# Kernel tuning notes

Hardware: AMD Instinct MI355X
Metric: run time of the kernel (lower is better)

The kernel has to match this reference:

```python
import jax, jax.numpy as jnp
import numpy as np

B, N, H = 8, 2000, 64  # batch, num_nodes(=input_dim), hidden(num_gru_units)


def _laplacian_self_loop(a):
    # batched: norm = D^{-1/2} (A + I) D^{-1/2}
    m = a + jnp.eye(a.shape[-1], dtype=a.dtype)
    d_inv_sqrt = jnp.sum(m, axis=-1) ** -0.5  # (B, N)
    return d_inv_sqrt[..., :, None] * m * d_inv_sqrt[..., None, :]


def _graph_conv(inputs, hidden_flat, adj, windd, W2, b2, W3, b3, W, b, out_dim):
    b_, _, n = inputs.shape
    # dynamic wind-based adjacency
    wind_now = inputs[:, 2, :] * 360.0  # (B, N)
    direction = jnp.abs(windd[None, :, :] - wind_now[:, :, None])  # (B, N, N)
    direction = jnp.where(direction > 360.0, 180.0, direction)
    d1 = jnp.maximum(jnp.cos(direction * (jnp.pi / 180.0)), 0.0)
    a = d1 @ W2.T + b2 + (adj @ W3.T + b3)[None]  # (B, N, N)
    a1 = _laplacian_self_loop(jnp.maximum(a, 0.0))
    # graph conv: concat [x, h] then A @ [.] then Linear
    x = jnp.concatenate([inputs[:, 0, :, None], hidden_flat.reshape(b_, n, H)], axis=2)  # (B,N,H+1)
    y = jnp.einsum('bij,bjh->bih', a1, x) @ W.T + b  # (B, N, out_dim)
    return y.reshape(b_, n * out_dim)


def reference(inputs, hidden_state, adj, windd, W2, b2, W3, b3, W1a, b1a, W1b, b1b, Wca1, Wca2, Wsa):
    b_, _, n = inputs.shape
    conc = _graph_conv(inputs, hidden_state, adj, windd, W2, b2, W3, b3, W1a, b1a, 2 * H)
    conc = conc.reshape(b_, 2 * H, n)  # faithful reshape (input_dim == N)
    # --- channel attention (CBAM) ---
    avg = jnp.mean(conc, axis=2, keepdims=True)  # (B, 2H, 1)
    mx = jnp.max(conc, axis=2, keepdims=True)
    def fc(v):
        return jnp.einsum('oc,bcx->box', Wca2, jax.nn.relu(jnp.einsum('oc,bcx->box', Wca1, v)))
    ca = jax.nn.sigmoid(fc(avg) + fc(mx))  # (B, 2H, 1)
    conc = ca * conc
    # --- spatial attention ---
    s = jnp.stack([jnp.mean(conc, axis=1), jnp.max(conc, axis=1)], axis=1)  # (B, 2, N)
    sa = jax.lax.conv_general_dilated(s, Wsa, window_strides=(1,), padding=((3, 3),),
                                      dimension_numbers=('NCH', 'OIH', 'NCH'))  # (B,1,N)
    conc = jax.nn.sigmoid(sa) * conc
    # --- GRU gates ---
    conc = jax.nn.sigmoid(conc.reshape(b_, 2 * H * n))
    r, u = jnp.split(conc, 2, axis=1)  # each (B, N*H)
    c = jnp.tanh(_graph_conv(inputs, r * hidden_state, adj, windd, W2, b2, W3, b3, W1b, b1b, H))
    new_hidden_state = u * hidden_state + (1.0 - u) * c
    return new_hidden_state


def setup_inputs() -> dict:
    key = jax.random.key(0)
    ks = jax.random.split(key, 12)
    inputs = jax.random.uniform(ks[0], (B, 3, N), dtype=jnp.float32)
    hidden_state = jax.random.normal(ks[1], (B, N * H), dtype=jnp.float32) * 0.1
    adj = jax.random.uniform(ks[2], (N, N), dtype=jnp.float32)
    windd = jax.random.uniform(ks[3], (N, N), dtype=jnp.float32) * 360.0
    sN = 1.0 / np.sqrt(N)
    W2 = jax.random.normal(ks[4], (N, N), dtype=jnp.float32) * sN
    b2 = jnp.zeros((N,), jnp.float32)
    W3 = jax.random.normal(ks[5], (N, N), dtype=jnp.float32) * sN
    b3 = jnp.zeros((N,), jnp.float32)
    sI = 1.0 / np.sqrt(H + 1)
    W1a = jax.random.normal(ks[6], (2 * H, H + 1), dtype=jnp.float32) * sI
    b1a = jnp.ones((2 * H,), jnp.float32)  # bias=1.0 in graph_conv1
    W1b = jax.random.normal(ks[7], (H, H + 1), dtype=jnp.float32) * sI
    b1b = jnp.zeros((H,), jnp.float32)
    Wca1 = jax.random.normal(ks[8], (2 * H // 16, 2 * H), dtype=jnp.float32) * (1.0 / np.sqrt(2 * H))
    Wca2 = jax.random.normal(ks[9], (2 * H, 2 * H // 16), dtype=jnp.float32) * (1.0 / np.sqrt(2 * H // 16))
    Wsa = jax.random.normal(ks[10], (1, 2, 7), dtype=jnp.float32) * (1.0 / np.sqrt(14))
    return {'inputs': inputs, 'hidden_state': hidden_state, 'adj': adj, 'windd': windd,
            'W2': W2, 'b2': b2, 'W3': W3, 'b3': b3, 'W1a': W1a, 'b1a': b1a,
            'W1b': W1b, 'b1b': b1b, 'Wca1': Wca1, 'Wca2': Wca2, 'Wsa': Wsa}
```

## Files before the change

### kernel.cpp

```cpp
#include <hip/hip_runtime.h>

#define NN 2000
#define BB 8
#define P  2048
#define NKT 64

typedef __attribute__((ext_vector_type(8))) short bf16x8;
typedef __attribute__((ext_vector_type(4))) float f32x4;

__device__ __forceinline__ float sigf(float x) { return 1.0f / (1.0f + expf(-x)); }

__device__ __forceinline__ short f2bf(float x) {
    union { float f; unsigned u; } v; v.f = x;
    unsigned r = v.u + 0x7fffu + ((v.u >> 16) & 1u);
    return (short)(r >> 16);
}
__device__ __forceinline__ float bf2f(short h) {
    union { unsigned u; float f; } v; v.u = ((unsigned)(unsigned short)h) << 16; return v.f;
}

__device__ __forceinline__ void gl2lds16(const short* g, short* l) {
    __builtin_amdgcn_global_load_lds(
        (const __attribute__((address_space(1))) void*)g,
        (__attribute__((address_space(3))) void*)l, 16, 0, 0);
}

__global__ __launch_bounds__(256) void k_cvtW(
    const float* __restrict__ s0, const float* __restrict__ s1, const float* __restrict__ s2,
    short* __restrict__ d0, short* __restrict__ d1, short* __restrict__ d2)
{
    const int i = blockIdx.x, sel = blockIdx.y, t = threadIdx.x;
    const float* s = (sel == 0) ? s0 : (sel == 1) ? s1 : s2;
    short* d = ((sel == 0) ? d0 : (sel == 1) ? d1 : d2) + ((size_t)i) * P + t * 8;
    bf16x8 v;
#pragma unroll
    for (int e = 0; e < 8; ++e) v[e] = 0;
    if (i < NN && t < 250) {
        const float* p = s + (size_t)i * NN + t * 8;
        float4 x0 = *(const float4*)p;
        float4 x1 = *(const float4*)(p + 4);
        float a[8] = {x0.x,x0.y,x0.z,x0.w,x1.x,x1.y,x1.z,x1.w};
#pragma unroll
        for (int e = 0; e < 8; ++e) v[e] = f2bf(a[e]);
    }
    *(bf16x8*)d = v;
}

__global__ __launch_bounds__(256) void k_cvtD1(
    const float* __restrict__ windd, const float* __restrict__ inputs, short* __restrict__ d1bf)
{
    const int i = blockIdx.x, t = threadIdx.x;
    const bool live = (i < NN) && (t < 250);
    float a[8];
    if (live) {
        const float* p = windd + (size_t)i * NN + t * 8;
        float4 x0 = *(const float4*)p;
        float4 x1 = *(const float4*)(p + 4);
        a[0]=x0.x; a[1]=x0.y; a[2]=x0.z; a[3]=x0.w;
        a[4]=x1.x; a[5]=x1.y; a[6]=x1.z; a[7]=x1.w;
    }
#pragma unroll
    for (int b = 0; b < BB; ++b) {
        bf16x8 v;
#pragma unroll
        for (int e = 0; e < 8; ++e) v[e] = 0;
        if (live) {
            const float wn = inputs[(size_t)b * 3 * NN + 2 * NN + i] * 360.0f;
#pragma unroll
            for (int e = 0; e < 8; ++e) {
                float dd = fabsf(a[e] - wn);
                dd = (dd > 360.0f) ? 180.0f : dd;
                float c = __cosf(dd * 0.01745329251994329577f);
                v[e] = f2bf(fmaxf(c, 0.0f));
            }
        }
        *(bf16x8*)(d1bf + ((size_t)b * P + i) * P + t * 8) = v;
    }
}

__global__ __launch_bounds__(512, 2) void k_g4s(
    const short* __restrict__ d1bf, const short* __restrict__ W2bf,
    const float* __restrict__ b2, const short* __restrict__ adjw,
    short* __restrict__ m_bf)
{
    __shared__ char smem[131072];
    const int t = threadIdx.x;
    const int w = t >> 6, lane = t & 63;
    const int wm = w >> 2, wn = w & 3;
    const int lr = lane & 15, lq = lane >> 4;
    const int tile = blockIdx.x;
    const int b = blockIdx.y;
    const int i0 = (tile & 7) * 256;
    const int j0 = (tile >> 3) * 256;
    const short* A  = d1bf + (size_t)b * P * P;
    const short* Bm = W2bf;

    const int cA0 = w * 64 + lane, cA1 = cA0 + 512;
    const int rA0 = cA0 >> 2, rA1 = cA1 >> 2;
    const short* srcA0 = A + (size_t)(i0 + rA0) * P + (((cA0 & 3) ^ ((rA0 >> 2) & 3)) * 8);
    const short* srcA1 = A + (size_t)(i0 + rA1) * P + (((cA1 & 3) ^ ((rA1 >> 2) & 3)) * 8);
    const short* srcB0 = Bm + (size_t)(j0 + rA0) * P + (((cA0 & 3) ^ ((rA0 >> 2) & 3)) * 8);
    const short* srcB1 = Bm + (size_t)(j0 + rA1) * P + (((cA1 & 3) ^ ((rA1 >> 2) & 3)) * 8);

#define STAGE_A(slot, ktI) do {                                                   \
        gl2lds16(srcA0 + (ktI) * 32, (short*)(smem + (slot) * 16384 + w * 1024)); \
        gl2lds16(srcA1 + (ktI) * 32, (short*)(smem + (slot) * 16384 + 8192 + w * 1024)); } while (0)
#define STAGE_B(slot, ktI) do {                                                   \
        gl2lds16(srcB0 + (ktI) * 32, (short*)(smem + 65536 + (slot) * 16384 + w * 1024)); \
        gl2lds16(srcB1 + (ktI) * 32, (short*)(smem + 65536 + (slot) * 16384 + 8192 + w * 1024)); } while (0)

    const int fch = (lq ^ (lr >> 2)) << 4;
    const int arowB = (wm * 128 + lr) * 64 + fch;
    const int browB = (wn * 64 + lr) * 64 + fch;

    f32x4 acc[8][4];
#pragma unroll
    for (int m = 0; m < 8; ++m)
#pragma unroll
        for (int n = 0; n < 4; ++n) acc[m][n] = (f32x4){0.f, 0.f, 0.f, 0.f};
    bf16x8 aF[4], bF[4];

    STAGE_A(0, 0); STAGE_B(0, 0);
    STAGE_A(1, 1); STAGE_B(1, 1);
    STAGE_A(2, 2); STAGE_B(2, 2);
    asm volatile("s_waitcnt vmcnt(0)" ::: "memory");
    __builtin_amdgcn_s_barrier();
    asm volatile("" ::: "memory");

#define MFMA_(a_, b_, m, n) acc[m][n] = __builtin_amdgcn_mfma_f32_16x16x32_bf16(a_, b_, acc[m][n], 0, 0, 0)
#define PHASE_MID()                                      \
    __builtin_amdgcn_s_barrier();                        \
    asm volatile("s_waitcnt lgkmcnt(0)" ::: "memory");   \
    __builtin_amdgcn_sched_barrier(0);                   \
    __builtin_amdgcn_s_setprio(1)
#define PHASE_TAIL()                                     \
    __builtin_amdgcn_s_setprio(0);                       \
    __builtin_amdgcn_sched_barrier(0);                   \
    asm volatile("s_waitcnt vmcnt(8)" ::: "memory");     \
    __builtin_amdgcn_s_barrier();                        \
    asm volatile("" ::: "memory")

    for (int kt = 0; kt < NKT; ++kt) {
        char* curA = smem + (kt & 3) * 16384;
        char* curB = smem + 65536 + (kt & 3) * 16384;
        const int stgSlot = (kt + 3) & 3;
        const int stgKt = (kt + 3 < NKT) ? (kt + 3) : (NKT - 1);

#pragma unroll
        for (int m = 0; m < 4; ++m) aF[m] = *(const bf16x8*)(curA + arowB + m * 1024);
#pragma unroll
        for (int n = 0; n < 4; ++n) bF[n] = *(const bf16x8*)(curB + browB + n * 1024);
        STAGE_A(stgSlot, stgKt);
        PHASE_MID();
#pragma unroll
        for (int m = 0; m < 4; ++m)
#pragma unroll
            for (int n = 0; n < 4; ++n) MFMA_(aF[m], bF[n], m, n);
        PHASE_TAIL();

#pragma unroll
        for (int m = 0; m < 4; ++m) aF[m] = *(const bf16x8*)(curA + arowB + (m + 4) * 1024);
        STAGE_B(stgSlot, stgKt);
        PHASE_MID();
#pragma unroll
        for (int m = 0; m < 4; ++m)
#pragma unroll
            for (int n = 0; n < 4; ++n) MFMA_(aF[m], bF[n], m + 4, n);
        PHASE_TAIL();
    }
    asm volatile("s_waitcnt vmcnt(0)" ::: "memory");

    const int rbase = i0 + wm * 128 + lq * 4;
    const int cbase = j0 + wn * 64 + lr;
#pragma unroll
    for (int m = 0; m < 8; ++m) {
#pragma unroll
        for (int n = 0; n < 4; ++n) {
            const int col = cbase + n * 16;
#pragma unroll
            for (int q = 0; q < 4; ++q) {
                const int row = rbase + m * 16 + q;
                short o = 0;
                if (row < NN && col < NN) {
                    float x = acc[m][n][q] + b2[col] + bf2f(adjw[(size_t)row * NN + col]);
                    x = fmaxf(x, 0.0f);
                    if (row == col) x += 1.0f;
                    o = f2bf(x);
                }
                m_bf[((size_t)b * P + row) * P + col] = o;
            }
        }
    }
#undef MFMA_
#undef PHASE_MID
#undef PHASE_TAIL
#undef STAGE_A
#undef STAGE_B
}

template<int EPI, int OUTD>
__global__ __launch_bounds__(256) void k_mfma(
    const short* __restrict__ Abase, const short* __restrict__ Bbase,
    const float* __restrict__ bias, const short* __restrict__ adjw,
    void* __restrict__ Cout, float* __restrict__ part, size_t aBatch)
{
    __shared__ short shA[4096];
    __shared__ short shB[4096];
    const int t = threadIdx.x;
    const int w = t >> 6, lane = t & 63;
    const int wr = w >> 1, wc = w & 1;

    int i0, j0, b, kt = 0;
    if (EPI == 2) {
        i0 = blockIdx.x * 128; j0 = 0; kt = blockIdx.y; b = blockIdx.z;
    } else {
        i0 = blockIdx.x * 128; j0 = blockIdx.y * 128; b = 0;
    }
    const int kb = (EPI == 2) ? kt * (P / 4) : 0;
    const int ke = (EPI == 2) ? kt * (P / 4) + (P / 4) : P;

    const short* A  = Abase + (size_t)b * aBatch;
    const short* Bm = Bbase + ((EPI == 2) ? (size_t)b * 128 * P : (size_t)0);

    f32x4 acc[4][4];
#pragma unroll
    for (int m = 0; m < 4; ++m)
#pragma unroll
        for (int n = 0; n < 4; ++n) acc[m][n] = (f32x4){0.f, 0.f, 0.f, 0.f};

    const int lidx0 = w * 128 + lane;
    const int lidx1 = lidx0 + 64;
    const short* aS0 = A  + (size_t)(i0 + (lidx0 >> 2)) * P + (lidx0 & 3) * 8;
    const short* aS1 = A  + (size_t)(i0 + (lidx1 >> 2)) * P + (lidx1 & 3) * 8;
    const short* bS0 = Bm + (size_t)(j0 + (lidx0 >> 2)) * P + (lidx0 & 3) * 8;
    const short* bS1 = Bm + (size_t)(j0 + (lidx1 >> 2)) * P + (lidx1 & 3) * 8;
    short* ldA0 = shA + (w * 128) * 8;
    short* ldA1 = shA + (w * 128 + 64) * 8;
    short* ldB0 = shB + (w * 128) * 8;
    short* ldB1 = shB + (w * 128 + 64) * 8;

    const int lr = lane & 15, lq = lane >> 4;
    const int aoff = (wr * 64 + lr) * 32 + lq * 8;
    const int boff = (wc * 64 + lr) * 32 + lq * 8;

    for (int k0 = kb; k0 < ke; k0 += 32) {
        gl2lds16(aS0 + k0, ldA0);
        gl2lds16(aS1 + k0, ldA1);
        gl2lds16(bS0 + k0, ldB0);
        gl2lds16(bS1 + k0, ldB1);
        __syncthreads();
        bf16x8 aF[4], bF[4];
#pragma unroll
        for (int m = 0; m < 4; ++m) aF[m] = *(const bf16x8*)(shA + aoff + m * 512);
#pragma unroll
        for (int n = 0; n < 4; ++n) bF[n] = *(const bf16x8*)(shB + boff + n * 512);
#pragma unroll
        for (int m = 0; m < 4; ++m)
#pragma unroll
            for (int n = 0; n < 4; ++n)
                acc[m][n] = __builtin_amdgcn_mfma_f32_16x16x32_bf16(aF[m], bF[n], acc[m][n], 0, 0, 0);
        __syncthreads();
    }

    const int rbase = i0 + wr * 64 + lq * 4;
    const int cbase = j0 + wc * 64 + lr;
#pragma unroll
    for (int m = 0; m < 4; ++m) {
#pragma unroll
        for (int n = 0; n < 4; ++n) {
            const int col = cbase + n * 16;
#pragma unroll
            for (int q = 0; q < 4; ++q) {
                const int row = rbase + m * 16 + q;
                float v = acc[m][n][q];
                if (EPI == 0) {
                    if (row < NN && col < NN)
                        ((short*)Cout)[(size_t)row * NN + col] = f2bf(v + bias[col]);
                } else {
                    if (row < NN && col < OUTD)
                        part[((size_t)(kt * BB + b) * NN + row) * OUTD + col] = v;
                }
            }
        }
    }
}

template<int OUTD>
__global__ __launch_bounds__(256) void k_comb(
    const float* __restrict__ part, const float* __restrict__ dinv,
    const float* __restrict__ bias, float* __restrict__ out)
{
    const size_t idx = (size_t)blockIdx.x * 256 + threadIdx.x;
    const size_t S = (size_t)BB * NN * OUTD;
    if (idx >= S) return;
    const int o = (int)(idx % OUTD);
    const size_t r = idx / OUTD;
    const int i = (int)(r % NN);
    const int b = (int)(r / NN);
    float s = ((part[idx] + part[idx + S]) + (part[idx + 2 * S] + part[idx + 3 * S]));
    out[idx] = s * dinv[b * NN + i] + bias[o];
}

__global__ __launch_bounds__(256) void k_rowsum_bf(const short* __restrict__ m_bf, float* __restrict__ dinv)
{
    const int i = blockIdx.x, b = blockIdx.y;
    const short* p = m_bf + ((size_t)b * P + i) * P + threadIdx.x * 8;
    bf16x8 v = *(const bf16x8*)p;
    float s = 0.0f;
#pragma unroll
    for (int e = 0; e < 8; ++e) s += bf2f(v[e]);
#pragma unroll
    for (int off = 32; off > 0; off >>= 1) s += __shfl_down(s, off);
    __shared__ float red[4];
    if ((threadIdx.x & 63) == 0) red[threadIdx.x >> 6] = s;
    __syncthreads();
    if (threadIdx.x == 0) dinv[b * NN + i] = rsqrtf(red[0] + red[1] + red[2] + red[3]);
}

template<int OUT>
__global__ __launch_bounds__(128) void k_xwT(
    const float* __restrict__ inputs, const float* __restrict__ hsrc,
    const float* __restrict__ W, const float* __restrict__ dinv, short* __restrict__ zT)
{
    const int b = blockIdx.y;
    const int j0 = blockIdx.x * 16;
    const int t = threadIdx.x;
    __shared__ float wl[128 * 65];
    __shared__ float xs[16 * 66];
    __shared__ float dj[16];
    for (int idx = t; idx < OUT * 65; idx += 128) wl[idx] = W[idx];
    for (int idx = t; idx < 16 * 64; idx += 128) {
        int jj = idx >> 6, hh = idx & 63, j = j0 + jj;
        xs[jj * 66 + 1 + hh] = (j < NN) ? hsrc[((size_t)b * NN + j) * 64 + hh] : 0.0f;
    }
    if (t < 16) {
        int j = j0 + t;
        xs[t * 66] = (j < NN) ? inputs[(size_t)b * 3 * NN + j] : 0.0f;
        dj[t] = (j < NN) ? dinv[b * NN + j] : 0.0f;
    }
    __syncthreads();
    for (int jj = 0; jj < 16; ++jj) {
        float a = 0.0f;
        if (t < OUT) {
            const float* xr = &xs[jj * 66];
            const float* wr = &wl[t * 65];
#pragma unroll
            for (int c = 0; c < 65; ++c) a = fmaf(xr[c], wr[c], a);
        }
        int j = j0 + jj;
        zT[((size_t)b * 128 + t) * P + j] = (t < OUT && j < NN) ? f2bf(a * dj[jj]) : (short)0;
    }
}

__global__ __launch_bounds__(256) void k_chred(const float* __restrict__ conc,
                                               float* __restrict__ avg, float* __restrict__ mx)
{
    const int bc = blockIdx.x;
    const float* p = conc + (size_t)bc * NN;
    float s = 0.0f, mv = -3.402823466e+38f;
    for (int n = threadIdx.x; n < NN; n += 256) { float v = p[n]; s += v; mv = fmaxf(mv, v); }
#pragma unroll
    for (int off = 32; off > 0; off >>= 1) {
        s += __shfl_down(s, off);
        mv = fmaxf(mv, __shfl_down(mv, off));
    }
    __shared__ float rs[4], rm[4];
    if ((threadIdx.x & 63) == 0) { rs[threadIdx.x >> 6] = s; rm[threadIdx.x >> 6] = mv; }
    __syncthreads();
    if (threadIdx.x == 0) {
        avg[bc] = (rs[0] + rs[1] + rs[2] + rs[3]) * (1.0f / NN);
        mx[bc]  = fmaxf(fmaxf(rm[0], rm[1]), fmaxf(rm[2], rm[3]));
    }
}

__global__ __launch_bounds__(128) void k_ca(
    const float* __restrict__ avg, const float* __restrict__ mx,
    const float* __restrict__ Wca1, const float* __restrict__ Wca2, float* __restrict__ ca)
{
    const int b = blockIdx.x, t = threadIdx.x;
    __shared__ float av[128], mv[128], h[16];
    av[t] = avg[b * 128 + t];
    mv[t] = mx[b * 128 + t];
    __syncthreads();
    if (t < 16) {
        int o8 = t & 7;
        const float* src = (t < 8) ? av : mv;
        float s = 0.0f;
        for (int c = 0; c < 128; ++c) s = fmaf(Wca1[o8 * 128 + c], src[c], s);
        h[t] = fmaxf(s, 0.0f);
    }
    __syncthreads();
    float s = 0.0f;
#pragma unroll
    for (int k = 0; k < 8; ++k) s = fmaf(Wca2[t * 8 + k], h[k] + h[8 + k], s);
    ca[b * 128 + t] = sigf(s);
}

__global__ __launch_bounds__(256) void k_satgate(
    const float* __restrict__ conc, const float* __restrict__ ca,
    const float* __restrict__ Wsa, const float* __restrict__ hidden,
    float* __restrict__ rh, float* __restrict__ u)
{
    const int b = blockIdx.y;
    const int n0 = blockIdx.x * 256;
    const int t = threadIdx.x;
    __shared__ float cas[128];
    __shared__ float wsa[14];
    __shared__ float s0l[262], s1l[262];
    if (t < 128) cas[t] = ca[b * 128 + t];
    if (t >= 128 && t < 142) wsa[t - 128] = Wsa[t - 128];
    __syncthreads();

    const float* cb = conc + (size_t)b * NN * 128;
    {
        const int n = n0 + t;
        float sm = 0.0f, sx = -3.402823466e+38f;
        if (n < NN) {
            for (int c = 0; c < 128; ++c) {
                float v = cas[c] * cb[(size_t)c * NN + n];
                sm += v; sx = fmaxf(sx, v);
            }
            s0l[t + 3] = sm * (1.0f / 128.0f);
            s1l[t + 3] = sx;
        } else { s0l[t + 3] = 0.0f; s1l[t + 3] = 0.0f; }
    }
    if (t < 6) {
        const int hn = (t < 3) ? (n0 - 3 + t) : (n0 + 256 + (t - 3));
        const int hi = (t < 3) ? t : (256 + t);
        float sm = 0.0f, sx = -3.402823466e+38f;
        if (hn >= 0 && hn < NN) {
            for (int c = 0; c < 128; ++c) {
                float v = cas[c] * cb[(size_t)c * NN + hn];
                sm += v; sx = fmaxf(sx, v);
            }
            s0l[hi] = sm * (1.0f / 128.0f);
            s1l[hi] = sx;
        } else { s0l[hi] = 0.0f; s1l[hi] = 0.0f; }
    }
    __syncthreads();

    const int n = n0 + t;
    if (n >= NN) return;
    float sa = 0.0f;
#pragma unroll
    for (int k = 0; k < 7; ++k)
        sa += wsa[k] * s0l[t + k] + wsa[7 + k] * s1l[t + k];
    float gs = sigf(sa);
    for (int c = 0; c < 128; ++c) {
        float v = gs * cas[c] * cb[(size_t)c * NN + n];
        float g = sigf(v);
        if (c < 64)
            rh[(size_t)b * NN * 64 + (size_t)c * NN + n] =
                g * hidden[(size_t)b * NN * 64 + (size_t)c * NN + n];
        else
            u[(size_t)b * NN * 64 + (size_t)(c - 64) * NN + n] = g;
    }
}

__global__ __launch_bounds__(256) void k_fin(
    const float* __restrict__ u, const float* __restrict__ hidden,
    const float* __restrict__ cpre, float* __restrict__ out)
{
    const size_t idx = (size_t)blockIdx.x * 256 + threadIdx.x;
    if (idx >= (size_t)BB * NN * 64) return;
    float uu = u[idx];
    out[idx] = uu * hidden[idx] + (1.0f - uu) * tanhf(cpre[idx]);
}

extern "C" void kernel_launch(void* const* d_in, const int* in_sizes, int n_in,
                              void* d_out, int out_size, void* d_ws, size_t ws_size,
                              hipStream_t stream)
{
    (void)in_sizes; (void)n_in; (void)out_size; (void)ws_size;
    const float* inputs = (const float*)d_in[0];
    const float* hidden = (const float*)d_in[1];
    const float* adj    = (const float*)d_in[2];
    const float* windd  = (const float*)d_in[3];
    const float* W2     = (const float*)d_in[4];
    const float* b2     = (const float*)d_in[5];
    const float* W3     = (const float*)d_in[6];
    const float* b3     = (const float*)d_in[7];
    const float* W1a    = (const float*)d_in[8];
    const float* b1a    = (const float*)d_in[9];
    const float* W1b    = (const float*)d_in[10];
    const float* b1b    = (const float*)d_in[11];
    const float* Wca1   = (const float*)d_in[12];
    const float* Wca2   = (const float*)d_in[13];
    const float* Wsa    = (const float*)d_in[14];
    float* out = (float*)d_out;

    char* W = (char*)d_ws;
    short* adjW3bf = (short*)(W + 0);
    short* W2bf    = (short*)(W + 8000000);
    short* W3bf    = (short*)(W + 16388608);
    short* adjbf   = (short*)(W + 24777216);
    short* m_bf    = (short*)(W + 16388608);
    char* D = W + 83497472;
    short* d1bf = (short*)D;
    float* dinv = (float*)(D + 0);
    float* avgb = (float*)(D + 64000);
    float* mxb  = (float*)(D + 68096);
    float* cab  = (float*)(D + 72192);
    short* zT   = (short*)(D + 204800);
    float* conc = (float*)(D + 4399104);
    float* rh   = (float*)(D + 12591104);
    float* ubuf = (float*)(D + 16687104);
    float* cpre = (float*)(D + 20783104);
    float* part = (float*)(D + 24879104);

    const size_t PP = (size_t)P * P;

    k_cvtW<<<dim3(P, 3), 256, 0, stream>>>(W2, W3, adj, W2bf, W3bf, adjbf);
    k_cvtD1<<<P, 256, 0, stream>>>(windd, inputs, d1bf);
    k_mfma<0, 0><<<dim3(16, 16, 1), 256, 0, stream>>>(adjbf, W3bf, b3, nullptr, adjW3bf, nullptr, 0);
    k_g4s<<<dim3(64, BB), 512, 0, stream>>>(d1bf, W2bf, b2, adjW3bf, m_bf);
    k_rowsum_bf<<<dim3(NN, BB), 256, 0, stream>>>(m_bf, dinv);
    k_xwT<128><<<dim3(128, BB), 128, 0, stream>>>(inputs, hidden, W1a, dinv, zT);
    k_mfma<2, 128><<<dim3(16, 4, BB), 256, 0, stream>>>(m_bf, zT, nullptr, nullptr, nullptr, part, PP);
    k_comb<128><<<(BB * NN * 128 + 255) / 256, 256, 0, stream>>>(part, dinv, b1a, conc);
    k_chred<<<BB * 128, 256, 0, stream>>>(conc, avgb, mxb);
    k_ca<<<BB, 128, 0, stream>>>(avgb, mxb, Wca1, Wca2, cab);
    k_satgate<<<dim3(8, BB), 256, 0, stream>>>(conc, cab, Wsa, hidden, rh, ubuf);
    k_xwT<64><<<dim3(128, BB), 128, 0, stream>>>(inputs, rh, W1b, dinv, zT);
    k_mfma<2, 64><<<dim3(16, 4, BB), 256, 0, stream>>>(m_bf, zT, nullptr, nullptr, nullptr, part, PP);
    k_comb<64><<<(BB * NN * 64 + 255) / 256, 256, 0, stream>>>(part, dinv, b1b, cpre);
    k_fin<<<(BB * NN * 64 + 255) / 256, 256, 0, stream>>>(ubuf, hidden, cpre, out);
}
```

Before: 442.4 us.

## Switch batched GEMM to double-buffered K=64 tiles with one barrier per step

The main batched d1@W2 GEMM now stages K=64 slices (twice as wide) into two LDS buffers instead of K=32 slices into a four-deep ring. The XOR swizzle is widened to 8 chunks to match. Each iteration issues two MFMAs per fragment pair and synchronises once with a full vmcnt(0) wait plus a barrier, replacing the two per-phase barrier pairs. The goal is to cut barrier and loop overhead per unit of work, at the cost of shallower prefetch that may expose global-load latency.

```diff
diff --git a/kernel.cpp b/kernel.cpp
--- a/kernel.cpp
+++ b/kernel.cpp
@@ -3,7 +3,7 @@
 #define NN 2000
 #define BB 8
 #define P  2048
-#define NKT 64
+#define NIT 32
 
 typedef __attribute__((ext_vector_type(8))) short bf16x8;
 typedef __attribute__((ext_vector_type(4))) float f32x4;
@@ -78,7 +78,7 @@
     }
 }
 
-__global__ __launch_bounds__(512, 2) void k_g4s(
+__global__ __launch_bounds__(512, 2) void k_gd(
     const short* __restrict__ d1bf, const short* __restrict__ W2bf,
     const float* __restrict__ b2, const short* __restrict__ adjw,
     short* __restrict__ m_bf)
@@ -95,80 +95,99 @@
     const short* A  = d1bf + (size_t)b * P * P;
     const short* Bm = W2bf;
 
-    const int cA0 = w * 64 + lane, cA1 = cA0 + 512;
-    const int rA0 = cA0 >> 2, rA1 = cA1 >> 2;
-    const short* srcA0 = A + (size_t)(i0 + rA0) * P + (((cA0 & 3) ^ ((rA0 >> 2) & 3)) * 8);
-    const short* srcA1 = A + (size_t)(i0 + rA1) * P + (((cA1 & 3) ^ ((rA1 >> 2) & 3)) * 8);
-    const short* srcB0 = Bm + (size_t)(j0 + rA0) * P + (((cA0 & 3) ^ ((rA0 >> 2) & 3)) * 8);
-    const short* srcB1 = Bm + (size_t)(j0 + rA1) * P + (((cA1 & 3) ^ ((rA1 >> 2) & 3)) * 8);
-
-#define STAGE_A(slot, ktI) do {                                                   \
-        gl2lds16(srcA0 + (ktI) * 32, (short*)(smem + (slot) * 16384 + w * 1024)); \
-        gl2lds16(srcA1 + (ktI) * 32, (short*)(smem + (slot) * 16384 + 8192 + w * 1024)); } while (0)
-#define STAGE_B(slot, ktI) do {                                                   \
-        gl2lds16(srcB0 + (ktI) * 32, (short*)(smem + 65536 + (slot) * 16384 + w * 1024)); \
-        gl2lds16(srcB1 + (ktI) * 32, (short*)(smem + 65536 + (slot) * 16384 + 8192 + w * 1024)); } while (0)
-
-    const int fch = (lq ^ (lr >> 2)) << 4;
-    const int arowB = (wm * 128 + lr) * 64 + fch;
-    const int browB = (wn * 64 + lr) * 64 + fch;
+    const short* srcA[4];
+    const short* srcB[4];
+#pragma unroll
+    for (int q = 0; q < 4; ++q) {
+        const int c = q * 512 + t;
+        const int r = c >> 3;
+        const int g = (c & 7) ^ (r & 7);
+        srcA[q] = A  + (size_t)(i0 + r) * P + g * 8;
+        srcB[q] = Bm + (size_t)(j0 + r) * P + g * 8;
+    }
+
+#define STAGE_A(slot, ktI) do {                                                        \
+        gl2lds16(srcA[0] + (ktI) * 64, (short*)(smem + (slot) * 32768 + (w * 64) * 16));          \
+        gl2lds16(srcA[1] + (ktI) * 64, (short*)(smem + (slot) * 32768 + (512 + w * 64) * 16));    \
+        gl2lds16(srcA[2] + (ktI) * 64, (short*)(smem + (slot) * 32768 + (1024 + w * 64) * 16));   \
+        gl2lds16(srcA[3] + (ktI) * 64, (short*)(smem + (slot) * 32768 + (1536 + w * 64) * 16)); } while (0)
+#define STAGE_B(slot, ktI) do {                                                        \
+        gl2lds16(srcB[0] + (ktI) * 64, (short*)(smem + 65536 + (slot) * 32768 + (w * 64) * 16));          \
+        gl2lds16(srcB[1] + (ktI) * 64, (short*)(smem + 65536 + (slot) * 32768 + (512 + w * 64) * 16));    \
+        gl2lds16(srcB[2] + (ktI) * 64, (short*)(smem + 65536 + (slot) * 32768 + (1024 + w * 64) * 16));   \
+        gl2lds16(srcB[3] + (ktI) * 64, (short*)(smem + 65536 + (slot) * 32768 + (1536 + w * 64) * 16)); } while (0)
+
+    const int fx0 = (lq << 4) ^ ((lr & 7) << 4);
+    const int fx1 = ((4 + lq) << 4) ^ ((lr & 7) << 4);
+    const int arowB = (wm * 128 + lr) * 128;
+    const int browB = (wn * 64 + lr) * 128;
 
     f32x4 acc[8][4];
 #pragma unroll
     for (int m = 0; m < 8; ++m)
 #pragma unroll
         for (int n = 0; n < 4; ++n) acc[m][n] = (f32x4){0.f, 0.f, 0.f, 0.f};
-    bf16x8 aF[4], bF[4];
-
-    STAGE_A(0, 0); STAGE_B(0, 0);
-    STAGE_A(1, 1); STAGE_B(1, 1);
-    STAGE_A(2, 2); STAGE_B(2, 2);
+    bf16x8 aF[4][2], bF[4][2];
+
+    STAGE_A(0, 0);
+    STAGE_B(0, 0);
     asm volatile("s_waitcnt vmcnt(0)" ::: "memory");
     __builtin_amdgcn_s_barrier();
     asm volatile("" ::: "memory");
 
 #define MFMA_(a_, b_, m, n) acc[m][n] = __builtin_amdgcn_mfma_f32_16x16x32_bf16(a_, b_, acc[m][n], 0, 0, 0)
-#define PHASE_MID()                                      \
-    __builtin_amdgcn_s_barrier();                        \
-    asm volatile("s_waitcnt lgkmcnt(0)" ::: "memory");   \
-    __builtin_amdgcn_sched_barrier(0);                   \
-    __builtin_amdgcn_s_setprio(1)
-#define PHASE_TAIL()                                     \
-    __builtin_amdgcn_s_setprio(0);                       \
-    __builtin_amdgcn_sched_barrier(0);                   \
-    asm volatile("s_waitcnt vmcnt(8)" ::: "memory");     \
-    __builtin_amdgcn_s_barrier();                        \
-    asm volatile("" ::: "memory")
-
-    for (int kt = 0; kt < NKT; ++kt) {
-        char* curA = smem + (kt & 3) * 16384;
-        char* curB = smem + 65536 + (kt & 3) * 16384;
-        const int stgSlot = (kt + 3) & 3;
-        const int stgKt = (kt + 3 < NKT) ? (kt + 3) : (NKT - 1);
-
-#pragma unroll
-        for (int m = 0; m < 4; ++m) aF[m] = *(const bf16x8*)(curA + arowB + m * 1024);
-#pragma unroll
-        for (int n = 0; n < 4; ++n) bF[n] = *(const bf16x8*)(curB + browB + n * 1024);
+
+    for (int kt = 0; kt < NIT; ++kt) {
+        char* curA = smem + (kt & 1) * 32768;
+        char* curB = smem + 65536 + (kt & 1) * 32768;
+        const int stgSlot = (kt + 1) & 1;
+        const int stgKt = (kt + 1 < NIT) ? (kt + 1) : (NIT - 1);
+
+#pragma unroll
+        for (int m = 0; m < 4; ++m) {
+            aF[m][0] = *(const bf16x8*)(curA + arowB + m * 2048 + fx0);
+            aF[m][1] = *(const bf16x8*)(curA + arowB + m * 2048 + fx1);
+        }
+#pragma unroll
+        for (int n = 0; n < 4; ++n) {
+            bF[n][0] = *(const bf16x8*)(curB + browB + n * 2048 + fx0);
+            bF[n][1] = *(const bf16x8*)(curB + browB + n * 2048 + fx1);
+        }
         STAGE_A(stgSlot, stgKt);
-        PHASE_MID();
+        asm volatile("s_waitcnt lgkmcnt(0)" ::: "memory");
+        __builtin_amdgcn_sched_barrier(0);
+        __builtin_amdgcn_s_setprio(1);
 #pragma unroll
         for (int m = 0; m < 4; ++m)
 #pragma unroll
-            for (int n = 0; n < 4; ++n) MFMA_(aF[m], bF[n], m, n);
-        PHASE_TAIL();
-
-#pragma unroll
-        for (int m = 0; m < 4; ++m) aF[m] = *(const bf16x8*)(curA + arowB + (m + 4) * 1024);
+            for (int n = 0; n < 4; ++n) {
+                MFMA_(aF[m][0], bF[n][0], m, n);
+                MFMA_(aF[m][1], bF[n][1], m, n);
+            }
+        __builtin_amdgcn_s_setprio(0);
+
+#pragma unroll
+        for (int m = 0; m < 4; ++m) {
+            aF[m][0] = *(const bf16x8*)(curA + arowB + (m + 4) * 2048 + fx0);
+            aF[m][1] = *(const bf16x8*)(curA + arowB + (m + 4) * 2048 + fx1);
+        }
         STAGE_B(stgSlot, stgKt);
-        PHASE_MID();
+        asm volatile("s_waitcnt lgkmcnt(0)" ::: "memory");
+        __builtin_amdgcn_sched_barrier(0);
+        __builtin_amdgcn_s_setprio(1);
 #pragma unroll
         for (int m = 0; m < 4; ++m)
 #pragma unroll
-            for (int n = 0; n < 4; ++n) MFMA_(aF[m], bF[n], m + 4, n);
-        PHASE_TAIL();
-    }
-    asm volatile("s_waitcnt vmcnt(0)" ::: "memory");
+            for (int n = 0; n < 4; ++n) {
+                MFMA_(aF[m][0], bF[n][0], m + 4, n);
+                MFMA_(aF[m][1], bF[n][1], m + 4, n);
+            }
+        __builtin_amdgcn_s_setprio(0);
+
+        asm volatile("s_waitcnt vmcnt(0)" ::: "memory");
+        __builtin_amdgcn_s_barrier();
+        asm volatile("" ::: "memory");
+    }
 
     const int rbase = i0 + wm * 128 + lq * 4;
     const int cbase = j0 + wn * 64 + lr;
@@ -192,8 +211,6 @@
         }
     }
 #undef MFMA_
-#undef PHASE_MID
-#undef PHASE_TAIL
 #undef STAGE_A
 #undef STAGE_B
 }
@@ -513,7 +530,7 @@
     k_cvtW<<<dim3(P, 3), 256, 0, stream>>>(W2, W3, adj, W2bf, W3bf, adjbf);
     k_cvtD1<<<P, 256, 0, stream>>>(windd, inputs, d1bf);
     k_mfma<0, 0><<<dim3(16, 16, 1), 256, 0, stream>>>(adjbf, W3bf, b3, nullptr, adjW3bf, nullptr, 0);
-    k_g4s<<<dim3(64, BB), 512, 0, stream>>>(d1bf, W2bf, b2, adjW3bf, m_bf);
+    k_gd<<<dim3(64, BB), 512, 0, stream>>>(d1bf, W2bf, b2, adjW3bf, m_bf);
     k_rowsum_bf<<<dim3(NN, BB), 256, 0, stream>>>(m_bf, dinv);
     k_xwT<128><<<dim3(128, BB), 128, 0, stream>>>(inputs, hidden, W1a, dinv, zT);
     k_mfma<2, 128><<<dim3(16, 4, BB), 256, 0, stream>>>(m_bf, zT, nullptr, nullptr, nullptr, part, PP);
```

Measured after the change: 420.0 us. -5.1%, faster.
